# Kernel optimization log

Measured on AMD Instinct MI355X. Metric: run time of the kernel, lower is better.

The kernel has to match this reference:

```python
import jax, jax.numpy as jnp
import numpy as np

N, C, D, K = 4096, 512, 64, 10  # samples, clusters (c_max), feature_dim, num_classes
KAPPA_N = 10.0


def setup_inputs() -> dict:
    key = jax.random.key(0)
    k1, k2, k3, k4, k5, k6 = jax.random.split(key, 6)
    data = jax.random.normal(k1, (N, D), dtype=jnp.float32)
    labels = jax.random.randint(k2, (N,), 0, K)
    # cluster support counts n >= kappa_n (mature clusters)
    n = jax.random.uniform(k3, (C,), dtype=jnp.float32) * 90.0 + KAPPA_N
    mu = jax.random.normal(k4, (C, D), dtype=jnp.float32) * 2.0
    # S is the scatter matrix; covariance Sigma = S / n must be SPD, so
    # build S = n * (0.1 * A A^T + 0.5 I)
    A = jax.random.normal(k5, (C, D, D), dtype=jnp.float32)
    AAT = jnp.einsum('cij,ckj->cik', A, A) / D
    S = n[:, None, None] * (0.1 * AAT + 0.5 * jnp.eye(D, dtype=jnp.float32))
    # one-hot class label per cluster
    cls = jax.random.randint(k6, (C,), 0, K)
    cluster_labels = jax.nn.one_hot(cls, K, dtype=jnp.int32)
    return {"data": data, "labels": labels, "n": n, "mu": mu, "S": S,
            "cluster_labels": cluster_labels}


def reference(data, labels, n, mu, S, cluster_labels):
    # Inference path of eGAUSSp.forward: for each sample z,
    #   Gamma_j = exp(-0.5 * (z - mu_j)^T (S_j / n_j)^{-1} (z - mu_j))   (all c clusters)
    #   scores  = defuzzify = sum_j Gamma_j * onehot(label_j) / sum_j Gamma_j
    # Vectorized over the batch (no cross-sample dependence in eval mode).
    eps = jnp.asarray(1e-6, data.dtype)
    Sigma = S / n[:, None, None] + eps * jnp.eye(S.shape[-1], dtype=data.dtype)  # [C,D,D]
    Sinv = jnp.linalg.inv(Sigma)                                                  # [C,D,D]
    diff = data[:, None, :] - mu[None, :, :]          # [N,C,D]
    tmp = jnp.einsum('ncd,cde->nce', diff, Sinv)      # [N,C,D]
    d2 = jnp.einsum('nce,nce->nc', tmp, diff)         # [N,C] squared Mahalanobis
    Gamma = jnp.exp(-0.5 * d2)                        # [N,C] activations
    lab_f = cluster_labels.astype(data.dtype)         # [C,K]
    scores = (Gamma @ lab_f) / (jnp.sum(Gamma, axis=1, keepdims=True) + 1e-12)  # [N,K]
    pred = jnp.argmax(scores, axis=1)
    clusters = jnp.argmax(Gamma, axis=1)
    return scores, pred, clusters
```

## Files before the change

kernel.cpp:

```cpp
#include <hip/hip_runtime.h>
#include <hip/hip_bf16.h>
#include <math.h>

#define NS 4096
#define NC 512
#define ND 64
#define NK 10
#define NPAIR 2080
#define KP 2176
#define BOFF 2080
#define KOFF 2144
#define KSPLIT 4
#define KT_PER (KP / 32 / KSPLIT)
#define ZB 1024
#define QB 2048

typedef __attribute__((ext_vector_type(8))) short short8;
typedef __attribute__((ext_vector_type(4))) float floatx4;

__device__ inline unsigned short f2b(float x) {
    __hip_bfloat16 h = __float2bfloat16(x);
    return __builtin_bit_cast(unsigned short, h);
}
__device__ inline float b2f(unsigned short u) {
    __hip_bfloat16 h = __builtin_bit_cast(__hip_bfloat16, u);
    return __bfloat162float(h);
}

__device__ inline float rlane(float v, int k) {
    return __builtin_bit_cast(float, __builtin_amdgcn_readlane(__builtin_bit_cast(int, v), k));
}

__device__ inline void gl16(const void* g, void* l) {
    __builtin_amdgcn_global_load_lds(
        (const __attribute__((address_space(1))) unsigned int*)g,
        (__attribute__((address_space(3))) unsigned int*)l, 16, 0, 0);
}

__global__ void table_kernel(uchar2* __restrict__ edt) {
    const int e = threadIdx.x;
    int off = e * 64 - (e * (e - 1)) / 2;
    for (int d = e; d < 64; ++d) edt[off + d - e] = make_uchar2(e, d);
    edt[BOFF + e] = make_uchar2(e, 64);
    if (e == 0) edt[KOFF] = make_uchar2(64, 64);
    if (e < KP - KOFF - 1) edt[KOFF + 1 + e] = make_uchar2(65, 65);
}

__global__ __launch_bounds__(256, 4) void prep_kernel(
    const float* __restrict__ data, const float* __restrict__ S,
    const float* __restrict__ n, const float* __restrict__ mu,
    const int* __restrict__ clab, const uchar2* __restrict__ edt,
    unsigned short* __restrict__ Qh, unsigned short* __restrict__ Ql,
    unsigned short* __restrict__ Bph, unsigned short* __restrict__ Bpl,
    float* __restrict__ d2, float* __restrict__ labf)
{
    __shared__ float AcolS[ND * (ND + 1)];
    __shared__ float cbuf[ND];
    __shared__ float rowbuf[2][ND];
    __shared__ float kksS[1];
    __shared__ float zq[2][66];

    if (blockIdx.x >= NC + ZB) {
        const int qb = blockIdx.x - (NC + ZB);
        const int half = threadIdx.x >> 7;
        const int i = threadIdx.x & 127;
        const int row = qb * 2 + half;
        if (i < 64) zq[half][i] = data[(size_t)row * ND + i];
        else if (i == 64) { zq[half][64] = 1.0f; zq[half][65] = 0.0f; }
        __syncthreads();
        const float* __restrict__ zr = zq[half];
        unsigned short* __restrict__ qh = Qh + (size_t)row * KP;
        unsigned short* __restrict__ ql = Ql + (size_t)row * KP;
        #pragma unroll
        for (int t = 0; t < 17; ++t) {
            const int p = t * 128 + i;
            const uchar2 ed = edt[p];
            const float v = zr[ed.x] * zr[ed.y];
            const unsigned short h = f2b(v);
            const unsigned short l = f2b(v - b2f(h));
            qh[p] = h;
            ql[p] = l;
        }
        return;
    }

    if (blockIdx.x >= NC) {
        const size_t base = (size_t)(blockIdx.x - NC) * 2048 + threadIdx.x * 8;
        *(float4*)&d2[base]     = make_float4(0.f, 0.f, 0.f, 0.f);
        *(float4*)&d2[base + 4] = make_float4(0.f, 0.f, 0.f, 0.f);
        return;
    }

    const int c = blockIdx.x;
    const int tid = threadIdx.x;
    const int j = tid & 63;
    const int w = tid >> 6;
    const int rbase = w * 16;

    const float inv_nc = 1.0f / n[c];
    const float* __restrict__ Sc = S + (size_t)c * ND * ND + j;

    float4 B0, B1, B2, B3;
#define LOADR(u) {                                                   \
    const float x0 = Sc[(rbase + 4*(u) + 0) * ND] * inv_nc;          \
    const float x1 = Sc[(rbase + 4*(u) + 1) * ND] * inv_nc;          \
    const float x2 = Sc[(rbase + 4*(u) + 2) * ND] * inv_nc;          \
    const float x3 = Sc[(rbase + 4*(u) + 3) * ND] * inv_nc;          \
    B##u.x = (rbase + 4*(u) + 0 == j) ? x0 + 1e-6f : x0;             \
    B##u.y = (rbase + 4*(u) + 1 == j) ? x1 + 1e-6f : x1;             \
    B##u.z = (rbase + 4*(u) + 2 == j) ? x2 + 1e-6f : x2;             \
    B##u.w = (rbase + 4*(u) + 3 == j) ? x3 + 1e-6f : x3; }
    LOADR(0) LOADR(1) LOADR(2) LOADR(3)
#undef LOADR

#define UPD4(u, K) {                                                  \
    const float c0 = rlane(B##u.x, K);                                \
    const float c1 = rlane(B##u.y, K);                                \
    const float c2 = rlane(B##u.z, K);                                \
    const float c3 = rlane(B##u.w, K);                                \
    B##u.x = (om && (4*(u)+0 == ((K)&15))) ? rowk : B##u.x * am - c0 * rowk; \
    B##u.y = (om && (4*(u)+1 == ((K)&15))) ? rowk : B##u.y * am - c1 * rowk; \
    B##u.z = (om && (4*(u)+2 == ((K)&15))) ? rowk : B##u.z * am - c2 * rowk; \
    B##u.w = (om && (4*(u)+3 == ((K)&15))) ? rowk : B##u.w * am - c3 * rowk; \
}
#define STEPC(TL, C, K) {                                             \
    if (w == ((K) >> 4)) {                                            \
        const float rp = B##TL.C;          \
        const float pv = rlane(rp, K);             \
        const float ip = 1.0f / pv;                                   \
        rowbuf[(K) & 1][j] = (j == (K)) ? ip : rp * ip;               \
    }                                                                 \
    __syncthreads();                                                  \
    const float rowk = rowbuf[(K) & 1][j];                            \
    const float am = (j == (K)) ? 0.0f : 1.0f;                        \
    const bool om = (w == ((K) >> 4));                                \
    UPD4(0, K) UPD4(1, K) UPD4(2, K) UPD4(3, K)                       \
}
#define STEP4(T, TL) STEPC(TL, x, 4*(T)+0) STEPC(TL, y, 4*(T)+1) \
                     STEPC(TL, z, 4*(T)+2) STEPC(TL, w, 4*(T)+3)
#define FOR16P(M) M(0,0) M(1,1) M(2,2) M(3,3) M(4,0) M(5,1) M(6,2) M(7,3) \
                  M(8,0) M(9,1) M(10,2) M(11,3) M(12,0) M(13,1) M(14,2) M(15,3)
    FOR16P(STEP4)
#undef FOR16P
#undef STEP4
#undef STEPC
#undef UPD4

#define MIR(u) *(float4*)&AcolS[j * (ND + 1) + rbase + 4*(u)] = B##u;
    MIR(0) MIR(1) MIR(2) MIR(3)
#undef MIR
    __syncthreads();

    if (w == 0) {
        const float* __restrict__ muc = mu + (size_t)c * ND;
        float y = 0.f;
        #pragma unroll
        for (int t = 0; t < 16; ++t) {
            const float4 v = *(const float4*)&AcolS[j * (ND + 1) + 4 * t];
            y += v.x * muc[4*t]     + v.y * muc[4*t + 1]
               + v.z * muc[4*t + 2] + v.w * muc[4*t + 3];
        }
        cbuf[j] = -2.0f * y;
        float kk = muc[j] * y;
        #pragma unroll
        for (int off = 32; off > 0; off >>= 1) kk += __shfl_down(kk, off);
        if (j == 0) {
            kksS[0] = kk;
            int lab = 0;
            for (int q = 0; q < NK; ++q) if (clab[c * NK + q] != 0) lab = q;
            labf[c] = (float)lab;
        }
    }
    __syncthreads();
    const float kks = kksS[0];

    unsigned short* __restrict__ ph = Bph + (size_t)c * KP;
    unsigned short* __restrict__ pl = Bpl + (size_t)c * KP;
    #pragma unroll
    for (int i = 0; i < 9; ++i) {
        const int t = w + 4 * i;
        if (t < KP / 64) {
            const int p = t * 64 + j;
            float val;
            if (p < NPAIR) {
                const uchar2 ed = edt[p];
                val = (ed.x == ed.y) ? AcolS[ed.x * (ND + 1) + ed.x]
                    : (AcolS[ed.y * (ND + 1) + ed.x] + AcolS[ed.x * (ND + 1) + ed.y]);
            } else if (p < KOFF) val = cbuf[p - BOFF];
            else if (p == KOFF)  val = kks;
            else                 val = 0.f;
            const unsigned short h = f2b(val);
            const unsigned short l = f2b(val - b2f(h));
            ph[p] = h;
            pl[p] = l;
        }
    }
}

__global__ __launch_bounds__(256, 2) void gemm_kernel(
    const unsigned short* __restrict__ Qh, const unsigned short* __restrict__ Ql,
    const unsigned short* __restrict__ Bph, const unsigned short* __restrict__ Bpl,
    float* __restrict__ d2)
{
    __shared__ unsigned short AhS[2][64 * 32], AlS[2][64 * 32];
    __shared__ unsigned short BhS[2][256 * 32], BlS[2][256 * 32];

    const int tid  = threadIdx.x;
    const int lane = tid & 63, w = tid >> 6;
    const int quad = lane >> 4, rlo = lane & 15;

    const int lid = blockIdx.x + 64 * blockIdx.y + 128 * blockIdx.z;
    const int nyz = lid & 7;
    const int m0 = (lid >> 3) * 64;
    const int n0 = (nyz & 1) * 256;
    const int koff0 = (nyz >> 1) * KT_PER * 32;

    const int srow = tid >> 2;
    const int sswz = (tid & 3) ^ ((srow >> 2) & 3);
    const unsigned short* aGh = Qh + (size_t)(m0 + srow) * KP + koff0 + sswz * 8;
    const unsigned short* aGl = Ql + (size_t)(m0 + srow) * KP + koff0 + sswz * 8;
    const unsigned short* bGh[4];
    const unsigned short* bGl[4];
    #pragma unroll
    for (int rd = 0; rd < 4; ++rd) {
        const size_t off = (size_t)(n0 + rd * 64 + srow) * KP + koff0 + sswz * 8;
        bGh[rd] = Bph + off;
        bGl[rd] = Bpl + off;
    }
    const int swz8 = (quad ^ ((rlo >> 2) & 3)) * 8;

    floatx4 acc[4][4] = {};

#define STAGE(b, t) {                                                 \
        const int _ko = (t) * 32;                                     \
        gl16(aGh + _ko, &AhS[b][tid * 8]);                            \
        gl16(aGl + _ko, &AlS[b][tid * 8]);                            \
        _Pragma("unroll")                                             \
        for (int rd = 0; rd < 4; ++rd) {                              \
            gl16(bGh[rd] + _ko, &BhS[b][(rd * 256 + tid) * 8]);       \
            gl16(bGl[rd] + _ko, &BlS[b][(rd * 256 + tid) * 8]);       \
        } }

    STAGE(0, 0)
    STAGE(1, 1)
    asm volatile("s_waitcnt vmcnt(10)" ::: "memory");
    __builtin_amdgcn_s_barrier();

    for (int kt = 0; kt < KT_PER; ++kt) {
        const int cur = kt & 1;

        short8 ah[4], al[4], bh[4], bl[4];
        #pragma unroll
        for (int i = 0; i < 4; ++i) {
            ah[i] = *(const short8*)&AhS[cur][(i * 16 + rlo) * 32 + swz8];
            al[i] = *(const short8*)&AlS[cur][(i * 16 + rlo) * 32 + swz8];
        }
        #pragma unroll
        for (int j2 = 0; j2 < 4; ++j2) {
            const int r = w * 64 + j2 * 16 + rlo;
            bh[j2] = *(const short8*)&BhS[cur][r * 32 + swz8];
            bl[j2] = *(const short8*)&BlS[cur][r * 32 + swz8];
        }
        asm volatile("s_waitcnt lgkmcnt(0)" ::: "memory");
        __builtin_amdgcn_sched_barrier(0);
        __builtin_amdgcn_s_barrier();

        if (kt < KT_PER - 2) STAGE(cur, kt + 2)

        __builtin_amdgcn_s_setprio(1);
        #pragma unroll
        for (int i = 0; i < 4; ++i)
            #pragma unroll
            for (int j2 = 0; j2 < 4; ++j2) {
                acc[i][j2] = __builtin_amdgcn_mfma_f32_16x16x32_bf16(al[i], bh[j2], acc[i][j2], 0, 0, 0);
                acc[i][j2] = __builtin_amdgcn_mfma_f32_16x16x32_bf16(ah[i], bl[j2], acc[i][j2], 0, 0, 0);
                acc[i][j2] = __builtin_amdgcn_mfma_f32_16x16x32_bf16(ah[i], bh[j2], acc[i][j2], 0, 0, 0);
            }
        __builtin_amdgcn_s_setprio(0);

        if (kt < KT_PER - 2) {
            asm volatile("s_waitcnt vmcnt(10)" ::: "memory");
        } else {
            asm volatile("s_waitcnt vmcnt(0)" ::: "memory");
        }
        __builtin_amdgcn_s_barrier();
    }
#undef STAGE

    #pragma unroll
    for (int i = 0; i < 4; ++i)
        #pragma unroll
        for (int j2 = 0; j2 < 4; ++j2) {
            const int m = m0 + i * 16 + quad * 4;
            const int nn = n0 + w * 64 + j2 * 16 + rlo;
            #pragma unroll
            for (int r = 0; r < 4; ++r)
                atomicAdd(&d2[(size_t)(m + r) * NC + nn], acc[i][j2][r]);
        }
}

__global__ __launch_bounds__(256) void score_kernel(
    const float* __restrict__ d2, const float* __restrict__ labf,
    float* __restrict__ out)
{
    const int s = blockIdx.x * 4 + (threadIdx.x >> 6);
    const int l = threadIdx.x & 63;

    float numer[NK];
    #pragma unroll
    for (int q = 0; q < NK; ++q) numer[q] = 0.f;
    float denom = 0.f, gmax = -1.f;
    int gidx = 0;

    #pragma unroll
    for (int i = 0; i < NC / 256; ++i) {
        const int c0 = i * 256 + l * 4;
        const float4 v = *(const float4*)&d2[(size_t)s * NC + c0];
        #pragma unroll
        for (int r = 0; r < 4; ++r) {
            const int c = c0 + r;
            const float G = __expf(-0.5f * ((const float*)&v)[r]);
            denom += G;
            const int lab = (int)labf[c];
            #pragma unroll
            for (int q = 0; q < NK; ++q) numer[q] += (q == lab) ? G : 0.f;
            if (G > gmax) { gmax = G; gidx = c; }
        }
    }

    #pragma unroll
    for (int off = 32; off > 0; off >>= 1) {
        const float og = __shfl_down(gmax, off);
        const int   oi = __shfl_down(gidx, off);
        if (og > gmax || (og == gmax && oi < gidx)) { gmax = og; gidx = oi; }
        denom += __shfl_down(denom, off);
        #pragma unroll
        for (int q = 0; q < NK; ++q) numer[q] += __shfl_down(numer[q], off);
    }

    if (l == 0) {
        const float inv = 1.0f / (denom + 1e-12f);
        float best = -1.f; int pk = 0;
        #pragma unroll
        for (int q = 0; q < NK; ++q) {
            const float sc = numer[q] * inv;
            out[(size_t)s * NK + q] = sc;
            if (sc > best) { best = sc; pk = q; }
        }
        out[(size_t)NS * NK + s]      = (float)pk;
        out[(size_t)NS * NK + NS + s] = (float)gidx;
    }
}

extern "C" void kernel_launch(void* const* d_in, const int* in_sizes, int n_in,
                              void* d_out, int out_size, void* d_ws, size_t ws_size,
                              hipStream_t stream)
{
    const float* data = (const float*)d_in[0];
    const float* n    = (const float*)d_in[2];
    const float* mu   = (const float*)d_in[3];
    const float* S    = (const float*)d_in[4];
    const int*   clab = (const int*)d_in[5];

    char* w = (char*)d_ws;
    unsigned short* Qh  = (unsigned short*)(w);
    unsigned short* Ql  = (unsigned short*)(w + 17825792);
    unsigned short* Bph = (unsigned short*)(w + 35651584);
    unsigned short* Bpl = (unsigned short*)(w + 37879808);
    float* d2   = (float*)(w + 40108032);
    float* labf = (float*)(w + 48496640);
    uchar2* edt = (uchar2*)(w + 48498688);

    hipLaunchKernelGGL(table_kernel, dim3(1), dim3(64), 0, stream, edt);
    hipLaunchKernelGGL(prep_kernel,  dim3(NC + ZB + QB), dim3(256), 0, stream,
                       data, S, n, mu, clab, edt, Qh, Ql, Bph, Bpl, d2, labf);
    hipLaunchKernelGGL(gemm_kernel,  dim3(NS / 64, NC / 256, KSPLIT), dim3(256), 0, stream,
                       Qh, Ql, Bph, Bpl, d2);
    hipLaunchKernelGGL(score_kernel, dim3(NS / 4), dim3(256), 0, stream,
                       d2, labf, (float*)d_out);
}
```

Before: 150.7 us.

## Load GEMM operands directly from global into double-buffered registers, bypassing LDS

The split-bf16 GEMM no longer stages A and B tiles through double-buffered shared memory with global_load_lds and barriers. Each wave now reads its MFMA fragments straight from global memory into two alternating register sets, overlapping the next k-step's loads with the current MFMAs. The low-half arrays are reached through fixed offsets from the high-half pointers, which assumes Ql and Bpl sit contiguously after Qh and Bph in memory. This removes LDS traffic and block barriers, but the four waves of a block now each fetch the shared A tile separately. Each row access is also only 64 contiguous bytes, so global access is less coalesced.

```diff
diff --git a/kernel.cpp b/kernel.cpp
--- a/kernel.cpp
+++ b/kernel.cpp
@@ -15,6 +15,9 @@
 #define ZB 1024
 #define QB 2048
 
+#define QLOFF 8912896ull
+#define BLOFF 1114112ull
+
 typedef __attribute__((ext_vector_type(8))) short short8;
 typedef __attribute__((ext_vector_type(4))) float floatx4;
 
@@ -29,12 +32,6 @@
 
 __device__ inline float rlane(float v, int k) {
     return __builtin_bit_cast(float, __builtin_amdgcn_readlane(__builtin_bit_cast(int, v), k));
-}
-
-__device__ inline void gl16(const void* g, void* l) {
-    __builtin_amdgcn_global_load_lds(
-        (const __attribute__((address_space(1))) unsigned int*)g,
-        (__attribute__((address_space(3))) unsigned int*)l, 16, 0, 0);
 }
 
 __global__ void table_kernel(uchar2* __restrict__ edt) {
@@ -202,9 +199,6 @@
     const unsigned short* __restrict__ Bph, const unsigned short* __restrict__ Bpl,
     float* __restrict__ d2)
 {
-    __shared__ unsigned short AhS[2][64 * 32], AlS[2][64 * 32];
-    __shared__ unsigned short BhS[2][256 * 32], BlS[2][256 * 32];
-
     const int tid  = threadIdx.x;
     const int lane = tid & 63, w = tid >> 6;
     const int quad = lane >> 4, rlo = lane & 15;
@@ -215,77 +209,53 @@
     const int n0 = (nyz & 1) * 256;
     const int koff0 = (nyz >> 1) * KT_PER * 32;
 
-    const int srow = tid >> 2;
-    const int sswz = (tid & 3) ^ ((srow >> 2) & 3);
-    const unsigned short* aGh = Qh + (size_t)(m0 + srow) * KP + koff0 + sswz * 8;
-    const unsigned short* aGl = Ql + (size_t)(m0 + srow) * KP + koff0 + sswz * 8;
-    const unsigned short* bGh[4];
-    const unsigned short* bGl[4];
-    #pragma unroll
-    for (int rd = 0; rd < 4; ++rd) {
-        const size_t off = (size_t)(n0 + rd * 64 + srow) * KP + koff0 + sswz * 8;
-        bGh[rd] = Bph + off;
-        bGl[rd] = Bpl + off;
-    }
-    const int swz8 = (quad ^ ((rlo >> 2) & 3)) * 8;
+    const size_t kbase = (size_t)koff0 + quad * 8;
+    const unsigned short* aH[4];
+    const unsigned short* bH[4];
+    #pragma unroll
+    for (int i = 0; i < 4; ++i)
+        aH[i] = Qh + (size_t)(m0 + i * 16 + rlo) * KP + kbase;
+    #pragma unroll
+    for (int j2 = 0; j2 < 4; ++j2)
+        bH[j2] = Bph + (size_t)(n0 + w * 64 + j2 * 16 + rlo) * KP + kbase;
 
     floatx4 acc[4][4] = {};
 
-#define STAGE(b, t) {                                                 \
-        const int _ko = (t) * 32;                                     \
-        gl16(aGh + _ko, &AhS[b][tid * 8]);                            \
-        gl16(aGl + _ko, &AlS[b][tid * 8]);                            \
+    short8 ahA[4], alA[4], bhA[4], blA[4];
+    short8 ahB[4], alB[4], bhB[4], blB[4];
+
+#define LOADSET(S, KO) {                                              \
+    _Pragma("unroll")                                                 \
+    for (int i = 0; i < 4; ++i) {                                     \
+        ah##S[i] = *(const short8*)(aH[i] + (KO));                    \
+        al##S[i] = *(const short8*)(aH[i] + QLOFF + (KO));            \
+        bh##S[i] = *(const short8*)(bH[i] + (KO));                    \
+        bl##S[i] = *(const short8*)(bH[i] + BLOFF + (KO));            \
+    } }
+
+#define MFMASET(S) {                                                  \
+    __builtin_amdgcn_s_setprio(1);                                    \
+    _Pragma("unroll")                                                 \
+    for (int i = 0; i < 4; ++i)                                       \
         _Pragma("unroll")                                             \
-        for (int rd = 0; rd < 4; ++rd) {                              \
-            gl16(bGh[rd] + _ko, &BhS[b][(rd * 256 + tid) * 8]);       \
-            gl16(bGl[rd] + _ko, &BlS[b][(rd * 256 + tid) * 8]);       \
-        } }
-
-    STAGE(0, 0)
-    STAGE(1, 1)
-    asm volatile("s_waitcnt vmcnt(10)" ::: "memory");
-    __builtin_amdgcn_s_barrier();
-
-    for (int kt = 0; kt < KT_PER; ++kt) {
-        const int cur = kt & 1;
-
-        short8 ah[4], al[4], bh[4], bl[4];
-        #pragma unroll
-        for (int i = 0; i < 4; ++i) {
-            ah[i] = *(const short8*)&AhS[cur][(i * 16 + rlo) * 32 + swz8];
-            al[i] = *(const short8*)&AlS[cur][(i * 16 + rlo) * 32 + swz8];
-        }
-        #pragma unroll
-        for (int j2 = 0; j2 < 4; ++j2) {
-            const int r = w * 64 + j2 * 16 + rlo;
-            bh[j2] = *(const short8*)&BhS[cur][r * 32 + swz8];
-            bl[j2] = *(const short8*)&BlS[cur][r * 32 + swz8];
-        }
-        asm volatile("s_waitcnt lgkmcnt(0)" ::: "memory");
-        __builtin_amdgcn_sched_barrier(0);
-        __builtin_amdgcn_s_barrier();
-
-        if (kt < KT_PER - 2) STAGE(cur, kt + 2)
-
-        __builtin_amdgcn_s_setprio(1);
-        #pragma unroll
-        for (int i = 0; i < 4; ++i)
-            #pragma unroll
-            for (int j2 = 0; j2 < 4; ++j2) {
-                acc[i][j2] = __builtin_amdgcn_mfma_f32_16x16x32_bf16(al[i], bh[j2], acc[i][j2], 0, 0, 0);
-                acc[i][j2] = __builtin_amdgcn_mfma_f32_16x16x32_bf16(ah[i], bl[j2], acc[i][j2], 0, 0, 0);
-                acc[i][j2] = __builtin_amdgcn_mfma_f32_16x16x32_bf16(ah[i], bh[j2], acc[i][j2], 0, 0, 0);
-            }
-        __builtin_amdgcn_s_setprio(0);
-
-        if (kt < KT_PER - 2) {
-            asm volatile("s_waitcnt vmcnt(10)" ::: "memory");
-        } else {
-            asm volatile("s_waitcnt vmcnt(0)" ::: "memory");
-        }
-        __builtin_amdgcn_s_barrier();
-    }
-#undef STAGE
+        for (int j2 = 0; j2 < 4; ++j2) {                              \
+            acc[i][j2] = __builtin_amdgcn_mfma_f32_16x16x32_bf16(al##S[i], bh##S[j2], acc[i][j2], 0, 0, 0); \
+            acc[i][j2] = __builtin_amdgcn_mfma_f32_16x16x32_bf16(ah##S[i], bl##S[j2], acc[i][j2], 0, 0, 0); \
+            acc[i][j2] = __builtin_amdgcn_mfma_f32_16x16x32_bf16(ah##S[i], bh##S[j2], acc[i][j2], 0, 0, 0); \
+        }                                                             \
+    __builtin_amdgcn_s_setprio(0); }
+
+    LOADSET(A, 0)
+    #pragma unroll 1
+    for (int kt = 0; kt < KT_PER - 1; kt += 2) {
+        LOADSET(B, (kt + 1) * 32)
+        MFMASET(A)
+        if (kt + 2 < KT_PER) LOADSET(A, (kt + 2) * 32)
+        MFMASET(B)
+    }
+    MFMASET(A)
+#undef LOADSET
+#undef MFMASET
 
     #pragma unroll
     for (int i = 0; i < 4; ++i)
```

Measured after the change: 183.0 us. 21.4% more time.

## Fuse scoring into GEMM via last-block counter and compute pair table inline

Applied to the files above, without the earlier changes.

Removes the separate table kernel by decoding the (e,d) pair index arithmetically with a sqrt-based inverse triangular formula. Fuses the score kernel into the GEMM epilogue: each of the 8 split/column blocks for a 64-row tile bumps an atomic counter, and the last one to finish computes scores for those rows. This cuts two kernel launches and a pass over the d2 buffer. In exchange, scoring runs on only 64 blocks with 16 rows per wave in series, so the tail of the GEMM may stretch out.

```diff
diff --git a/kernel.cpp b/kernel.cpp
--- a/kernel.cpp
+++ b/kernel.cpp
@@ -37,22 +37,27 @@
         (__attribute__((address_space(3))) unsigned int*)l, 16, 0, 0);
 }
 
-__global__ void table_kernel(uchar2* __restrict__ edt) {
-    const int e = threadIdx.x;
-    int off = e * 64 - (e * (e - 1)) / 2;
-    for (int d = e; d < 64; ++d) edt[off + d - e] = make_uchar2(e, d);
-    edt[BOFF + e] = make_uchar2(e, 64);
-    if (e == 0) edt[KOFF] = make_uchar2(64, 64);
-    if (e < KP - KOFF - 1) edt[KOFF + 1 + e] = make_uchar2(65, 65);
+__device__ inline uchar2 ed_decode(int p) {
+    if (p < NPAIR) {
+        const float s = sqrtf((float)(16641 - 8 * p));
+        int e = (int)((129.0f - s) * 0.5f);
+        int off = e * 64 - (e * (e - 1)) / 2;
+        const int offn = off + (64 - e);
+        if (p >= offn) { off = offn; ++e; }
+        else if (p < off) { off -= (65 - e); --e; }
+        return make_uchar2((unsigned char)e, (unsigned char)(e + (p - off)));
+    } else if (p < KOFF) return make_uchar2((unsigned char)(p - BOFF), 64);
+    else if (p == KOFF)  return make_uchar2(64, 64);
+    return make_uchar2(65, 65);
 }
 
 __global__ __launch_bounds__(256, 4) void prep_kernel(
     const float* __restrict__ data, const float* __restrict__ S,
     const float* __restrict__ n, const float* __restrict__ mu,
-    const int* __restrict__ clab, const uchar2* __restrict__ edt,
+    const int* __restrict__ clab,
     unsigned short* __restrict__ Qh, unsigned short* __restrict__ Ql,
     unsigned short* __restrict__ Bph, unsigned short* __restrict__ Bpl,
-    float* __restrict__ d2, float* __restrict__ labf)
+    float* __restrict__ d2, float* __restrict__ labf, int* __restrict__ ctr)
 {
     __shared__ float AcolS[ND * (ND + 1)];
     __shared__ float cbuf[ND];
@@ -74,7 +79,7 @@
         #pragma unroll
         for (int t = 0; t < 17; ++t) {
             const int p = t * 128 + i;
-            const uchar2 ed = edt[p];
+            const uchar2 ed = ed_decode(p);
             const float v = zr[ed.x] * zr[ed.y];
             const unsigned short h = f2b(v);
             const unsigned short l = f2b(v - b2f(h));
@@ -85,6 +90,7 @@
     }
 
     if (blockIdx.x >= NC) {
+        if (blockIdx.x == NC && threadIdx.x < 64) ctr[threadIdx.x] = 0;
         const size_t base = (size_t)(blockIdx.x - NC) * 2048 + threadIdx.x * 8;
         *(float4*)&d2[base]     = make_float4(0.f, 0.f, 0.f, 0.f);
         *(float4*)&d2[base + 4] = make_float4(0.f, 0.f, 0.f, 0.f);
@@ -183,7 +189,7 @@
             const int p = t * 64 + j;
             float val;
             if (p < NPAIR) {
-                const uchar2 ed = edt[p];
+                const uchar2 ed = ed_decode(p);
                 val = (ed.x == ed.y) ? AcolS[ed.x * (ND + 1) + ed.x]
                     : (AcolS[ed.y * (ND + 1) + ed.x] + AcolS[ed.x * (ND + 1) + ed.y]);
             } else if (p < KOFF) val = cbuf[p - BOFF];
@@ -200,7 +206,8 @@
 __global__ __launch_bounds__(256, 2) void gemm_kernel(
     const unsigned short* __restrict__ Qh, const unsigned short* __restrict__ Ql,
     const unsigned short* __restrict__ Bph, const unsigned short* __restrict__ Bpl,
-    float* __restrict__ d2)
+    float* __restrict__ d2, const float* __restrict__ labf,
+    int* __restrict__ ctr, float* __restrict__ out)
 {
     __shared__ unsigned short AhS[2][64 * 32], AlS[2][64 * 32];
     __shared__ unsigned short BhS[2][256 * 32], BlS[2][256 * 32];
@@ -297,58 +304,63 @@
             for (int r = 0; r < 4; ++r)
                 atomicAdd(&d2[(size_t)(m + r) * NC + nn], acc[i][j2][r]);
         }
-}
-
-__global__ __launch_bounds__(256) void score_kernel(
-    const float* __restrict__ d2, const float* __restrict__ labf,
-    float* __restrict__ out)
-{
-    const int s = blockIdx.x * 4 + (threadIdx.x >> 6);
-    const int l = threadIdx.x & 63;
-
-    float numer[NK];
-    #pragma unroll
-    for (int q = 0; q < NK; ++q) numer[q] = 0.f;
-    float denom = 0.f, gmax = -1.f;
-    int gidx = 0;
-
-    #pragma unroll
-    for (int i = 0; i < NC / 256; ++i) {
-        const int c0 = i * 256 + l * 4;
-        const float4 v = *(const float4*)&d2[(size_t)s * NC + c0];
-        #pragma unroll
-        for (int r = 0; r < 4; ++r) {
-            const int c = c0 + r;
-            const float G = __expf(-0.5f * ((const float*)&v)[r]);
-            denom += G;
-            const int lab = (int)labf[c];
-            #pragma unroll
-            for (int q = 0; q < NK; ++q) numer[q] += (q == lab) ? G : 0.f;
-            if (G > gmax) { gmax = G; gidx = c; }
-        }
-    }
-
-    #pragma unroll
-    for (int off = 32; off > 0; off >>= 1) {
-        const float og = __shfl_down(gmax, off);
-        const int   oi = __shfl_down(gidx, off);
-        if (og > gmax || (og == gmax && oi < gidx)) { gmax = og; gidx = oi; }
-        denom += __shfl_down(denom, off);
-        #pragma unroll
-        for (int q = 0; q < NK; ++q) numer[q] += __shfl_down(numer[q], off);
-    }
-
-    if (l == 0) {
-        const float inv = 1.0f / (denom + 1e-12f);
-        float best = -1.f; int pk = 0;
-        #pragma unroll
-        for (int q = 0; q < NK; ++q) {
-            const float sc = numer[q] * inv;
-            out[(size_t)s * NK + q] = sc;
-            if (sc > best) { best = sc; pk = q; }
-        }
-        out[(size_t)NS * NK + s]      = (float)pk;
-        out[(size_t)NS * NK + NS + s] = (float)gidx;
+
+    __threadfence();
+    __syncthreads();
+    volatile int* flag = (volatile int*)&AhS[0][0];
+    if (tid == 0) *flag = atomicAdd(&ctr[m0 >> 6], 1);
+    __syncthreads();
+    if (*flag != KSPLIT * 2 - 1) return;
+    __threadfence();
+
+    const int l = lane;
+    for (int it = 0; it < 16; ++it) {
+        const int s = m0 + w * 16 + it;
+
+        float numer[NK];
+        #pragma unroll
+        for (int q = 0; q < NK; ++q) numer[q] = 0.f;
+        float denom = 0.f, gmax = -1.f;
+        int gidx = 0;
+
+        #pragma unroll
+        for (int i = 0; i < NC / 256; ++i) {
+            const int c0 = i * 256 + l * 4;
+            const float4 v = *(const float4*)&d2[(size_t)s * NC + c0];
+            #pragma unroll
+            for (int r = 0; r < 4; ++r) {
+                const int c = c0 + r;
+                const float G = __expf(-0.5f * ((const float*)&v)[r]);
+                denom += G;
+                const int lab = (int)labf[c];
+                #pragma unroll
+                for (int q = 0; q < NK; ++q) numer[q] += (q == lab) ? G : 0.f;
+                if (G > gmax) { gmax = G; gidx = c; }
+            }
+        }
+
+        #pragma unroll
+        for (int off = 32; off > 0; off >>= 1) {
+            const float og = __shfl_down(gmax, off);
+            const int   oi = __shfl_down(gidx, off);
+            if (og > gmax || (og == gmax && oi < gidx)) { gmax = og; gidx = oi; }
+            denom += __shfl_down(denom, off);
+            #pragma unroll
+            for (int q = 0; q < NK; ++q) numer[q] += __shfl_down(numer[q], off);
+        }
+
+        if (l == 0) {
+            const float inv = 1.0f / (denom + 1e-12f);
+            float best = -1.f; int pk = 0;
+            #pragma unroll
+            for (int q = 0; q < NK; ++q) {
+                const float sc = numer[q] * inv;
+                out[(size_t)s * NK + q] = sc;
+                if (sc > best) { best = sc; pk = q; }
+            }
+            out[(size_t)NS * NK + s]      = (float)pk;
+            out[(size_t)NS * NK + NS + s] = (float)gidx;
+        }
     }
 }
 
@@ -369,13 +381,10 @@
     unsigned short* Bpl = (unsigned short*)(w + 37879808);
     float* d2   = (float*)(w + 40108032);
     float* labf = (float*)(w + 48496640);
-    uchar2* edt = (uchar2*)(w + 48498688);
-
-    hipLaunchKernelGGL(table_kernel, dim3(1), dim3(64), 0, stream, edt);
+    int*   ctr  = (int*)(w + 48498688);
+
     hipLaunchKernelGGL(prep_kernel,  dim3(NC + ZB + QB), dim3(256), 0, stream,
-                       data, S, n, mu, clab, edt, Qh, Ql, Bph, Bpl, d2, labf);
+                       data, S, n, mu, clab, Qh, Ql, Bph, Bpl, d2, labf, ctr);
     hipLaunchKernelGGL(gemm_kernel,  dim3(NS / 64, NC / 256, KSPLIT), dim3(256), 0, stream,
-                       Qh, Ql, Bph, Bpl, d2);
-    hipLaunchKernelGGL(score_kernel, dim3(NS / 4), dim3(256), 0, stream,
-                       d2, labf, (float*)d_out);
-}
+                       Qh, Ql, Bph, Bpl, d2, labf, ctr, (float*)d_out);
+}
```

Result: slower. 248.9 us (+65.2%).
